# Optimization experiments

Measured on AMD Instinct MI355X. Metric: run time of the kernel, lower is better.

The kernel has to match this reference:

```python
import jax, jax.numpy as jnp
import numpy as np

B, N, IN_DIM, DIM, HEADS = 2, 4096, 1024, 1024, 8
MAX_MASK = 2048
SCALE = DIM ** -0.5  # original uses full dim, not per-head dim


def setup_inputs() -> dict:
    key = jax.random.key(0)
    k_x, k_qkv, k_o, k_b, k_m = jax.random.split(key, 5)
    x = jax.random.normal(k_x, (B, N, IN_DIM), dtype=jnp.float32)
    W_qkv = jax.random.normal(k_qkv, (IN_DIM, 3 * DIM), dtype=jnp.float32) * 0.02
    W_out = jax.random.normal(k_o, (DIM, DIM), dtype=jnp.float32) * 0.02
    b_out = jax.random.normal(k_b, (DIM,), dtype=jnp.float32) * 0.02
    mask = jax.random.randint(k_m, (1, 1, MAX_MASK, MAX_MASK), 0, 2, dtype=jnp.int32)
    return {"x": x, "W_qkv": W_qkv, "W_out": W_out, "b_out": b_out,
            "mask": mask, "max_mask": MAX_MASK}


def reference(x, W_qkv, W_out, b_out, mask, max_mask):
    b, n, _ = x.shape
    d = DIM // HEADS
    qkv = x @ W_qkv                                   # [b, n, 3*dim]
    qkv = qkv.reshape(b, n, 3, HEADS, d).transpose(2, 0, 3, 1, 4)  # [3, b, h, n, d]
    q, k, v = qkv[0], qkv[1], qkv[2]
    dots = jnp.einsum('bhid,bhjd->bhij', q, k) * SCALE  # [b, h, n, n]
    # partial submatrix masking on the top-left [max_mask, max_mask] block
    m = max_mask
    sub = jnp.where(mask == 0, -jnp.inf, dots[:, :, :m, :m])
    dots = dots.at[:, :, :m, :m].set(sub)
    attn = jax.nn.softmax(dots, axis=-1)
    out = jnp.einsum('bhij,bhjd->bhid', attn, v)       # [b, h, n, d]
    out = out.transpose(0, 2, 1, 3).reshape(b, n, HEADS * d)
    return out @ W_out + b_out
```

## Files before the change

kernel.cpp:

```cpp
#include <hip/hip_runtime.h>
#include <hip/hip_bf16.h>
#include <stdint.h>


typedef __attribute__((ext_vector_type(8))) short short8;
typedef __attribute__((ext_vector_type(4))) float f32x4;
typedef __attribute__((ext_vector_type(16))) float f32x16;
typedef unsigned int uint2v __attribute__((ext_vector_type(2)));

#define SCALE_Q 0.0450842200f

__device__ __forceinline__ unsigned short f2bf(float f) {
  union { float f; unsigned int u; } v;
  v.f = f;
  return (unsigned short)((v.u + 0x7fffu + ((v.u >> 16) & 1u)) >> 16);
}

__device__ __forceinline__ unsigned int pkbf2(float a, float b) {
  __hip_bfloat162 h = __float22bfloat162_rn(make_float2(a, b));
  union { __hip_bfloat162 h; unsigned int u; } c;
  c.h = h;
  return c.u;
}

__device__ __forceinline__ void gload_lds16(const void* g, void* l) {
  __builtin_amdgcn_global_load_lds(
      (const __attribute__((address_space(1))) uint32_t*)(uintptr_t)g,
      (__attribute__((address_space(3))) uint32_t*)(uintptr_t)l, 16, 0, 0);
}

__device__ __forceinline__ f32x4 zero4() {
  f32x4 z; z.x = 0.f; z.y = 0.f; z.z = 0.f; z.w = 0.f; return z;
}

__global__ __launch_bounds__(256) void k_cvt_x(const float* __restrict__ in,
                                               unsigned short* __restrict__ out) {
  const int t = blockIdx.x * 256 + threadIdx.x;
  const float4 v = ((const float4*)in)[t];
  ushort4 o;
  o.x = f2bf(v.x); o.y = f2bf(v.y); o.z = f2bf(v.z); o.w = f2bf(v.w);
  ((ushort4*)out)[t] = o;
}

__global__ __launch_bounds__(256) void k_cvt_wt(const float* __restrict__ w,
                                                unsigned short* __restrict__ wt,
                                                int Nn) {
  __shared__ float t[32][33];
  const int n0 = blockIdx.x << 5, k0 = blockIdx.y << 5;
  const int c = threadIdx.x & 31, r8 = threadIdx.x >> 5;
#pragma unroll
  for (int i = 0; i < 4; ++i) {
    const int r = (i << 3) + r8;
    t[r][c] = w[(long)(k0 + r) * Nn + n0 + c];
  }
  __syncthreads();
#pragma unroll
  for (int i = 0; i < 4; ++i) {
    const int r = (i << 3) + r8;
    wt[(long)(n0 + r) * 1024 + k0 + c] = f2bf(t[c][r]);
  }
}

__global__ __launch_bounds__(256) void k_mask_bits(
    const int* __restrict__ m, unsigned long long* __restrict__ mb) {
  const int t = blockIdx.x * 256 + threadIdx.x;
  const unsigned long long b = __ballot(m[t] != 0);
  if ((threadIdx.x & 63) == 0) mb[t >> 6] = b;
}

__global__ __launch_bounds__(256, 2) void k_qkv_gemm(
    const unsigned short* __restrict__ A,
    const unsigned short* __restrict__ Bt,
    unsigned short* __restrict__ Qs, unsigned short* __restrict__ Ks,
    unsigned short* __restrict__ Vt) {
  __shared__ __align__(16) unsigned short lA[8][128][8];
  __shared__ __align__(16) unsigned short lB[8][128][8];
  const int tid = threadIdx.x;
  const int w = tid >> 6, ln = tid & 63;
  const int m15 = ln & 15, q4 = ln >> 4;
  const int wm = (w >> 1) << 6, wn = (w & 1) << 6;
  const int id = blockIdx.x;
  const int swz = (id & 7) * 192 + (id >> 3);
  const int tn = swz % 24, tm = swz / 24;
  const int which = tn >> 3;
  const int h = tn & 7;

  f32x4 acc[4][4];
#pragma unroll
  for (int i = 0; i < 4; ++i)
#pragma unroll
    for (int j = 0; j < 4; ++j) acc[i][j] = zero4();

#define QKV_STAGE()                                                       \
  {                                                                       \
    _Pragma("unroll")                                                     \
    for (int c = 0; c < 4; ++c) {                                         \
      const int p = ((c * 4 + w) << 10) + (ln << 4);                      \
      const int g = p >> 11;                                              \
      const int r = (p & 2047) >> 4;                                      \
      gload_lds16(A + ((long)tm * 128 + r) * 1024 + kb + g * 8,           \
                  (char*)&lA[0][0][0] + p);                               \
      gload_lds16(Bt + ((long)tn * 128 + r) * 1024 + kb + g * 8,          \
                  (char*)&lB[0][0][0] + p);                               \
    }                                                                     \
  }

  if (which == 2) {
    for (int kb = 0; kb < 1024; kb += 64) {
      __syncthreads();
      QKV_STAGE();
      __syncthreads();
#pragma unroll
      for (int kk = 0; kk < 2; ++kk) {
        short8 afr[4], bfr[4];
#pragma unroll
        for (int i = 0; i < 4; ++i)
          afr[i] = *(const short8*)&lA[kk * 4 + q4][wm + i * 16 + m15][0];
#pragma unroll
        for (int j = 0; j < 4; ++j)
          bfr[j] = *(const short8*)&lB[kk * 4 + q4][wn + j * 16 + m15][0];
#pragma unroll
        for (int i = 0; i < 4; ++i)
#pragma unroll
          for (int j = 0; j < 4; ++j)
            acc[i][j] = __builtin_amdgcn_mfma_f32_16x16x32_bf16(
                afr[i], bfr[j], acc[i][j], 0, 0, 0);
      }
    }
#pragma unroll
    for (int i = 0; i < 4; ++i) {
      const int m0 = (tm << 7) + wm + (i << 4) + (q4 << 2);
      const int b = m0 >> 12, row0 = m0 & 4095;
#pragma unroll
      for (int j = 0; j < 4; ++j) {
        const int dd = wn + (j << 4) + m15;
        const long bh = b * 8 + h;
        uint2 u;
        u.x = pkbf2(acc[i][j][0], acc[i][j][1]);
        u.y = pkbf2(acc[i][j][2], acc[i][j][3]);
        *(uint2*)&Vt[(bh * 128 + dd) * 4096 + row0] = u;
      }
    }
  } else {
    for (int kb = 0; kb < 1024; kb += 64) {
      __syncthreads();
      QKV_STAGE();
      __syncthreads();
#pragma unroll
      for (int kk = 0; kk < 2; ++kk) {
        short8 afr[4], bfr[4];
#pragma unroll
        for (int i = 0; i < 4; ++i)
          afr[i] = *(const short8*)&lA[kk * 4 + q4][wm + i * 16 + m15][0];
#pragma unroll
        for (int j = 0; j < 4; ++j)
          bfr[j] = *(const short8*)&lB[kk * 4 + q4][wn + j * 16 + m15][0];
#pragma unroll
        for (int i = 0; i < 4; ++i)
#pragma unroll
          for (int j = 0; j < 4; ++j)
            acc[i][j] = __builtin_amdgcn_mfma_f32_16x16x32_bf16(
                bfr[j], afr[i], acc[i][j], 0, 0, 0);
      }
    }
    unsigned short* Dst = (which == 0) ? Qs : Ks;
    const float sc = (which == 0) ? SCALE_Q : 1.0f;
#pragma unroll
    for (int i = 0; i < 4; ++i) {
      const int m = (tm << 7) + wm + (i << 4) + m15;
      const int b = m >> 12, row = m & 4095;
      const long bh = b * 8 + h;
#pragma unroll
      for (int j = 0; j < 4; ++j) {
        const int dd0 = wn + (j << 4) + (q4 << 2);
        uint2 u;
        u.x = pkbf2(acc[i][j][0] * sc, acc[i][j][1] * sc);
        u.y = pkbf2(acc[i][j][2] * sc, acc[i][j][3] * sc);
        *(uint2*)&Dst[(bh * 4096 + row) * 128 + dd0] = u;
      }
    }
  }
#undef QKV_STAGE
}

__global__ __launch_bounds__(256, 2) void k_flash(
    const unsigned short* __restrict__ Qs, const unsigned short* __restrict__ Ks,
    const unsigned short* __restrict__ Vt,
    const unsigned long long* __restrict__ mbits,
    unsigned short* __restrict__ Ob) {
  __shared__ __align__(16) unsigned short lK[2][16][64][8];
  __shared__ __align__(16) unsigned short lV[2][8][128][8];

  const int tid = threadIdx.x;
  const int w = tid >> 6, ln = tid & 63;
  const int l31 = ln & 31, hi = ln >> 5, hi4 = hi << 2;
  const bool hib = hi != 0;
  (void)hib;
  const int id = blockIdx.x;
  const int xcd = id & 7, jj = id >> 3;
  const int bh = (xcd << 1) | (jj >> 5);
  const int rowblk = jj & 31;
  const int rbase = rowblk * 128 + w * 32;
  const int qrow = rbase + l31;

  const unsigned short* Qbh = Qs + (long)bh * 524288;
  const unsigned short* Kbh = Ks + (long)bh * 524288;
  const unsigned short* Vbh = Vt + (long)bh * 524288;

  short8 qf[8];
#pragma unroll
  for (int ks = 0; ks < 8; ++ks)
    qf[ks] = *(const short8*)(Qbh + (long)qrow * 128 + ks * 16 + hi * 8);

  f32x16 o[4];
#pragma unroll
  for (int d = 0; d < 4; ++d)
#pragma unroll
    for (int r = 0; r < 16; ++r) o[d][r] = 0.f;
  float lacc = 0.f;

  const bool maskblk = rowblk < 16;

#define STAGE_KV(dst, kvoff)                                              \
  {                                                                       \
    _Pragma("unroll")                                                     \
    for (int c = 0; c < 4; ++c) {                                         \
      const int p = ((c * 4 + w) << 10) + (ln << 4);                      \
      const int cs = p >> 10;                                             \
      const int j = (p & 1023) >> 4;                                      \
      gload_lds16(Kbh + (long)((kvoff) + j) * 128 + cs * 8,               \
                  (char*)&lK[dst][0][0][0] + p);                          \
    }                                                                     \
    _Pragma("unroll")                                                     \
    for (int c = 0; c < 4; ++c) {                                         \
      const int p = ((c * 4 + w) << 10) + (ln << 4);                      \
      const int cv = p >> 11;                                             \
      const int dv = (p & 2047) >> 4;                                     \
      gload_lds16(Vbh + (long)dv * 4096 + (kvoff) + cv * 8,               \
                  (char*)&lV[dst][0][0][0] + p);                          \
    }                                                                     \
  }

#if __has_builtin(__builtin_amdgcn_permlane32_swap)
#define PLSWAP(a, b)                                                      \
  {                                                                       \
    uint2v r_ = __builtin_amdgcn_permlane32_swap((a), (b), false, false); \
    (a) = r_[0]; (b) = r_[1];                                             \
  }
#else
#define PLSWAP(a, b)                                                      \
  {                                                                       \
    const unsigned pa_ = (unsigned)__shfl_xor((int)(a), 32);              \
    const unsigned pb_ = (unsigned)__shfl_xor((int)(b), 32);              \
    const unsigned na_ = hib ? pb_ : (a);                                 \
    const unsigned nb_ = hib ? (b) : pa_;                                 \
    (a) = na_; (b) = nb_;                                                 \
  }
#endif

  STAGE_KV(0, 0);
  __syncthreads();

  int cur = 0;
  for (int kv = 0; kv < 4096; kv += 64) {
    unsigned long long mw = 0ull;
    const bool domask = maskblk && (kv < 2048);
    if (domask) mw = mbits[(long)qrow * 32 + (kv >> 6)];

    const int nb = cur ^ 1;
    if (kv + 64 < 4096) STAGE_KV(nb, kv + 64);

    f32x16 s0, s1;
#pragma unroll
    for (int r = 0; r < 16; ++r) { s0[r] = 0.f; s1[r] = 0.f; }
    __builtin_amdgcn_s_setprio(1);
#pragma unroll
    for (int ks = 0; ks < 8; ++ks) {
      const short8 kf0 = *(const short8*)&lK[cur][ks * 2 + hi][l31][0];
      const short8 kf1 = *(const short8*)&lK[cur][ks * 2 + hi][32 + l31][0];
      s0 = __builtin_amdgcn_mfma_f32_32x32x16_bf16(kf0, qf[ks], s0, 0, 0, 0);
      s1 = __builtin_amdgcn_mfma_f32_32x32x16_bf16(kf1, qf[ks], s1, 0, 0, 0);
    }
    __builtin_amdgcn_s_setprio(0);

    if (domask) {
      const unsigned mlo = ((unsigned)mw) >> hi4;
      const unsigned mhi = ((unsigned)(mw >> 32)) >> hi4;
#pragma unroll
      for (int r = 0; r < 16; ++r) {
        const int c = ((r >> 2) << 3) + (r & 3);
        if (!((mlo >> c) & 1u)) s0[r] = -1e30f;
        if (!((mhi >> c) & 1u)) s1[r] = -1e30f;
      }
    }

    float p0[16], p1[16];
#pragma unroll
    for (int r = 0; r < 16; ++r) {
      p0[r] = __builtin_amdgcn_exp2f(s0[r]);
      p1[r] = __builtin_amdgcn_exp2f(s1[r]);
      lacc += p0[r] + p1[r];
    }

    unsigned w00 = pkbf2(p0[0], p0[1]),   w01 = pkbf2(p0[2], p0[3]);
    unsigned w10 = pkbf2(p0[4], p0[5]),   w11 = pkbf2(p0[6], p0[7]);
    PLSWAP(w00, w10); PLSWAP(w01, w11);
    unsigned w20 = pkbf2(p0[8], p0[9]),   w21 = pkbf2(p0[10], p0[11]);
    unsigned w30 = pkbf2(p0[12], p0[13]), w31 = pkbf2(p0[14], p0[15]);
    PLSWAP(w20, w30); PLSWAP(w21, w31);
    unsigned x00 = pkbf2(p1[0], p1[1]),   x01 = pkbf2(p1[2], p1[3]);
    unsigned x10 = pkbf2(p1[4], p1[5]),   x11 = pkbf2(p1[6], p1[7]);
    PLSWAP(x00, x10); PLSWAP(x01, x11);
    unsigned x20 = pkbf2(p1[8], p1[9]),   x21 = pkbf2(p1[10], p1[11]);
    unsigned x30 = pkbf2(p1[12], p1[13]), x31 = pkbf2(p1[14], p1[15]);
    PLSWAP(x20, x30); PLSWAP(x21, x31);

    union { unsigned u[4]; short8 s; } pa0, pa1, pa2, pa3;
    pa0.u[0] = w00; pa0.u[1] = w01; pa0.u[2] = w10; pa0.u[3] = w11;
    pa1.u[0] = w20; pa1.u[1] = w21; pa1.u[2] = w30; pa1.u[3] = w31;
    pa2.u[0] = x00; pa2.u[1] = x01; pa2.u[2] = x10; pa2.u[3] = x11;
    pa3.u[0] = x20; pa3.u[1] = x21; pa3.u[2] = x30; pa3.u[3] = x31;
    const short8 pa[4] = {pa0.s, pa1.s, pa2.s, pa3.s};

    __builtin_amdgcn_s_setprio(1);
#pragma unroll
    for (int ksl = 0; ksl < 4; ++ksl) {
#pragma unroll
      for (int db = 0; db < 4; ++db) {
        const short8 vf =
            *(const short8*)&lV[cur][ksl * 2 + hi][db * 32 + l31][0];
        o[db] = __builtin_amdgcn_mfma_f32_32x32x16_bf16(pa[ksl], vf,
                                                        o[db], 0, 0, 0);
      }
    }
    __builtin_amdgcn_s_setprio(0);

    __syncthreads();
    cur = nb;
  }
#undef STAGE_KV
#undef PLSWAP

  const float lh = lacc + __shfl_xor(lacc, 32);
  const float linv = 1.0f / lh;

  const int b = bh >> 3, h = bh & 7;
#pragma unroll
  for (int r = 0; r < 16; ++r) {
    const int qr = (r & 3) + ((r >> 2) << 3) + hi4;
    const float li = __shfl(linv, qr);
    const int row = rbase + qr;
    unsigned short* op = Ob + ((long)(b * 4096 + row)) * 1024 + h * 128 + l31;
#pragma unroll
    for (int db = 0; db < 4; ++db)
      op[db * 32] = f2bf(o[db][r] * li);
  }
}

__global__ __launch_bounds__(256, 2) void k_proj_gemm(
    const unsigned short* __restrict__ A,
    const unsigned short* __restrict__ Bt,
    const float* __restrict__ bias, float* __restrict__ Out) {
  __shared__ __align__(16) unsigned short lA[8][128][8];
  __shared__ __align__(16) unsigned short lB[8][128][8];
  const int tid = threadIdx.x;
  const int w = tid >> 6, ln = tid & 63;
  const int m15 = ln & 15, q4 = ln >> 4;
  const int wm = (w >> 1) << 6, wn = (w & 1) << 6;
  const int id = blockIdx.x;
  const int swz = (id & 7) * 64 + (id >> 3);
  const int tn = swz & 7, tm = swz >> 3;

  f32x4 acc[4][4];
#pragma unroll
  for (int i = 0; i < 4; ++i)
#pragma unroll
    for (int j = 0; j < 4; ++j) acc[i][j] = zero4();

  for (int kb = 0; kb < 1024; kb += 64) {
    __syncthreads();
#pragma unroll
    for (int c = 0; c < 4; ++c) {
      const int p = ((c * 4 + w) << 10) + (ln << 4);
      const int g = p >> 11;
      const int r = (p & 2047) >> 4;
      gload_lds16(A + ((long)tm * 128 + r) * 1024 + kb + g * 8,
                  (char*)&lA[0][0][0] + p);
      gload_lds16(Bt + ((long)tn * 128 + r) * 1024 + kb + g * 8,
                  (char*)&lB[0][0][0] + p);
    }
    __syncthreads();
#pragma unroll
    for (int kk = 0; kk < 2; ++kk) {
      short8 afr[4], bfr[4];
#pragma unroll
      for (int i = 0; i < 4; ++i)
        afr[i] = *(const short8*)&lA[kk * 4 + q4][wm + i * 16 + m15][0];
#pragma unroll
      for (int j = 0; j < 4; ++j)
        bfr[j] = *(const short8*)&lB[kk * 4 + q4][wn + j * 16 + m15][0];
#pragma unroll
      for (int i = 0; i < 4; ++i)
#pragma unroll
        for (int j = 0; j < 4; ++j)
          acc[i][j] = __builtin_amdgcn_mfma_f32_16x16x32_bf16(
              afr[i], bfr[j], acc[i][j], 0, 0, 0);
    }
  }

#pragma unroll
  for (int i = 0; i < 4; ++i)
#pragma unroll
    for (int r = 0; r < 4; ++r) {
      const int m = (tm << 7) + wm + (i << 4) + (q4 << 2) + r;
#pragma unroll
      for (int j = 0; j < 4; ++j) {
        const int n = (tn << 7) + wn + (j << 4) + m15;
        Out[(long)m * 1024 + n] = acc[i][j][r] + bias[n];
      }
    }
}

extern "C" void kernel_launch(void* const* d_in, const int* in_sizes, int n_in,
                              void* d_out, int out_size, void* d_ws,
                              size_t ws_size, hipStream_t stream) {
  const float* x = (const float*)d_in[0];
  const float* Wqkv = (const float*)d_in[1];
  const float* Wout = (const float*)d_in[2];
  const float* bout = (const float*)d_in[3];
  const int* mask = (const int*)d_in[4];
  float* out = (float*)d_out;

  char* ws = (char*)d_ws;
  unsigned short* xb     = (unsigned short*)(ws);
  unsigned short* wqkv_t = (unsigned short*)(ws + 16777216);
  unsigned short* wout_t = (unsigned short*)(ws + 23068672);
  unsigned short* Qs     = (unsigned short*)(ws + 25165824);
  unsigned short* Ks     = (unsigned short*)(ws + 41943040);
  unsigned short* Vt     = (unsigned short*)(ws + 58720256);
  unsigned short* Ob     = xb;
  unsigned long long* mbits = (unsigned long long*)wqkv_t;

  hipLaunchKernelGGL(k_cvt_x, dim3(8192), dim3(256), 0, stream, x, xb);
  hipLaunchKernelGGL(k_cvt_wt, dim3(96, 32), dim3(256), 0, stream, Wqkv, wqkv_t, 3072);
  hipLaunchKernelGGL(k_cvt_wt, dim3(32, 32), dim3(256), 0, stream, Wout, wout_t, 1024);
  hipLaunchKernelGGL(k_qkv_gemm, dim3(1536), dim3(256), 0, stream,
                     xb, wqkv_t, Qs, Ks, Vt);
  hipLaunchKernelGGL(k_mask_bits, dim3(16384), dim3(256), 0, stream,
                     mask, mbits);
  hipLaunchKernelGGL(k_flash, dim3(512), dim3(256), 0, stream,
                     Qs, Ks, Vt, mbits, Ob);
  hipLaunchKernelGGL(k_proj_gemm, dim3(512), dim3(256), 0, stream,
                     Ob, wout_t, bout, out);
}
```

Before: 431.2 us.

## Double-buffer GEMM LDS tiles, split flash PV into halves, merge prep kernels

Three conversion kernels are merged into one launch to cut launch overhead. Both the QKV and projection GEMMs now double-buffer their LDS tiles, prefetching the next K slice while MFMAs run on the current one, which drops one barrier per iteration. In the flash kernel, the softmax/exp/pack of the second 32-column half is interleaved with the PV MFMAs of the first half, so VALU work can overlap matrix work. Doubling LDS per GEMM block may lower occupancy under launch_bounds(256,2).

Result: no change. 426.2 us (-1.2%).

```diff
diff --git a/kernel.cpp b/kernel.cpp
--- a/kernel.cpp
+++ b/kernel.cpp
@@ -33,31 +33,43 @@
   f32x4 z; z.x = 0.f; z.y = 0.f; z.z = 0.f; z.w = 0.f; return z;
 }
 
-__global__ __launch_bounds__(256) void k_cvt_x(const float* __restrict__ in,
-                                               unsigned short* __restrict__ out) {
-  const int t = blockIdx.x * 256 + threadIdx.x;
-  const float4 v = ((const float4*)in)[t];
-  ushort4 o;
-  o.x = f2bf(v.x); o.y = f2bf(v.y); o.z = f2bf(v.z); o.w = f2bf(v.w);
-  ((ushort4*)out)[t] = o;
-}
-
-__global__ __launch_bounds__(256) void k_cvt_wt(const float* __restrict__ w,
-                                                unsigned short* __restrict__ wt,
-                                                int Nn) {
+__global__ __launch_bounds__(256) void k_prep(
+    const float* __restrict__ x, unsigned short* __restrict__ xb,
+    const float* __restrict__ Wqkv, unsigned short* __restrict__ wqkv_t,
+    const float* __restrict__ Wout, unsigned short* __restrict__ wout_t) {
   __shared__ float t[32][33];
-  const int n0 = blockIdx.x << 5, k0 = blockIdx.y << 5;
-  const int c = threadIdx.x & 31, r8 = threadIdx.x >> 5;
-#pragma unroll
-  for (int i = 0; i < 4; ++i) {
-    const int r = (i << 3) + r8;
-    t[r][c] = w[(long)(k0 + r) * Nn + n0 + c];
-  }
-  __syncthreads();
-#pragma unroll
-  for (int i = 0; i < 4; ++i) {
-    const int r = (i << 3) + r8;
-    wt[(long)(n0 + r) * 1024 + k0 + c] = f2bf(t[c][r]);
+  const int id = blockIdx.x;
+  const int tid = threadIdx.x;
+  if (id < 8192) {
+    const int i = id * 256 + tid;
+    const float4 v = ((const float4*)x)[i];
+    ushort4 o;
+    o.x = f2bf(v.x); o.y = f2bf(v.y); o.z = f2bf(v.z); o.w = f2bf(v.w);
+    ((ushort4*)xb)[i] = o;
+  } else {
+    const float* w;
+    unsigned short* wt;
+    int Nn, bx, by;
+    if (id < 11264) {
+      const int r = id - 8192;
+      w = Wqkv; wt = wqkv_t; Nn = 3072; bx = r % 96; by = r / 96;
+    } else {
+      const int r = id - 11264;
+      w = Wout; wt = wout_t; Nn = 1024; bx = r % 32; by = r / 32;
+    }
+    const int n0 = bx << 5, k0 = by << 5;
+    const int c = tid & 31, r8 = tid >> 5;
+#pragma unroll
+    for (int i = 0; i < 4; ++i) {
+      const int r = (i << 3) + r8;
+      t[r][c] = w[(long)(k0 + r) * Nn + n0 + c];
+    }
+    __syncthreads();
+#pragma unroll
+    for (int i = 0; i < 4; ++i) {
+      const int r = (i << 3) + r8;
+      wt[(long)(n0 + r) * 1024 + k0 + c] = f2bf(t[c][r]);
+    }
   }
 }
 
@@ -73,8 +85,8 @@
     const unsigned short* __restrict__ Bt,
     unsigned short* __restrict__ Qs, unsigned short* __restrict__ Ks,
     unsigned short* __restrict__ Vt) {
-  __shared__ __align__(16) unsigned short lA[8][128][8];
-  __shared__ __align__(16) unsigned short lB[8][128][8];
+  __shared__ __align__(16) unsigned short lA[2][8][128][8];
+  __shared__ __align__(16) unsigned short lB[2][8][128][8];
   const int tid = threadIdx.x;
   const int w = tid >> 6, ln = tid & 63;
   const int m15 = ln & 15, q4 = ln >> 4;
@@ -91,34 +103,37 @@
 #pragma unroll
     for (int j = 0; j < 4; ++j) acc[i][j] = zero4();
 
-#define QKV_STAGE()                                                       \
+#define QKV_STAGE(buf, kb)                                                \
   {                                                                       \
     _Pragma("unroll")                                                     \
     for (int c = 0; c < 4; ++c) {                                         \
       const int p = ((c * 4 + w) << 10) + (ln << 4);                      \
       const int g = p >> 11;                                              \
       const int r = (p & 2047) >> 4;                                      \
-      gload_lds16(A + ((long)tm * 128 + r) * 1024 + kb + g * 8,           \
-                  (char*)&lA[0][0][0] + p);                               \
-      gload_lds16(Bt + ((long)tn * 128 + r) * 1024 + kb + g * 8,          \
-                  (char*)&lB[0][0][0] + p);                               \
+      gload_lds16(A + ((long)tm * 128 + r) * 1024 + (kb) + g * 8,         \
+                  (char*)&lA[buf][0][0][0] + p);                          \
+      gload_lds16(Bt + ((long)tn * 128 + r) * 1024 + (kb) + g * 8,        \
+                  (char*)&lB[buf][0][0][0] + p);                          \
     }                                                                     \
   }
 
+  QKV_STAGE(0, 0);
+  __syncthreads();
+
+  int cur = 0;
   if (which == 2) {
     for (int kb = 0; kb < 1024; kb += 64) {
-      __syncthreads();
-      QKV_STAGE();
-      __syncthreads();
+      const int nb2 = cur ^ 1;
+      if (kb + 64 < 1024) QKV_STAGE(nb2, kb + 64);
 #pragma unroll
       for (int kk = 0; kk < 2; ++kk) {
         short8 afr[4], bfr[4];
 #pragma unroll
         for (int i = 0; i < 4; ++i)
-          afr[i] = *(const short8*)&lA[kk * 4 + q4][wm + i * 16 + m15][0];
+          afr[i] = *(const short8*)&lA[cur][kk * 4 + q4][wm + i * 16 + m15][0];
 #pragma unroll
         for (int j = 0; j < 4; ++j)
-          bfr[j] = *(const short8*)&lB[kk * 4 + q4][wn + j * 16 + m15][0];
+          bfr[j] = *(const short8*)&lB[cur][kk * 4 + q4][wn + j * 16 + m15][0];
 #pragma unroll
         for (int i = 0; i < 4; ++i)
 #pragma unroll
@@ -126,6 +141,8 @@
             acc[i][j] = __builtin_amdgcn_mfma_f32_16x16x32_bf16(
                 afr[i], bfr[j], acc[i][j], 0, 0, 0);
       }
+      __syncthreads();
+      cur = nb2;
     }
 #pragma unroll
     for (int i = 0; i < 4; ++i) {
@@ -143,18 +160,17 @@
     }
   } else {
     for (int kb = 0; kb < 1024; kb += 64) {
-      __syncthreads();
-      QKV_STAGE();
-      __syncthreads();
+      const int nb2 = cur ^ 1;
+      if (kb + 64 < 1024) QKV_STAGE(nb2, kb + 64);
 #pragma unroll
       for (int kk = 0; kk < 2; ++kk) {
         short8 afr[4], bfr[4];
 #pragma unroll
         for (int i = 0; i < 4; ++i)
-          afr[i] = *(const short8*)&lA[kk * 4 + q4][wm + i * 16 + m15][0];
+          afr[i] = *(const short8*)&lA[cur][kk * 4 + q4][wm + i * 16 + m15][0];
 #pragma unroll
         for (int j = 0; j < 4; ++j)
-          bfr[j] = *(const short8*)&lB[kk * 4 + q4][wn + j * 16 + m15][0];
+          bfr[j] = *(const short8*)&lB[cur][kk * 4 + q4][wn + j * 16 + m15][0];
 #pragma unroll
         for (int i = 0; i < 4; ++i)
 #pragma unroll
@@ -162,6 +178,8 @@
             acc[i][j] = __builtin_amdgcn_mfma_f32_16x16x32_bf16(
                 bfr[j], afr[i], acc[i][j], 0, 0, 0);
       }
+      __syncthreads();
+      cur = nb2;
     }
     unsigned short* Dst = (which == 0) ? Qs : Ks;
     const float sc = (which == 0) ? SCALE_Q : 1.0f;
@@ -283,55 +301,72 @@
     }
     __builtin_amdgcn_s_setprio(0);
 
+    const unsigned mlo = ((unsigned)mw) >> hi4;
+    const unsigned mhi = ((unsigned)(mw >> 32)) >> hi4;
+
     if (domask) {
-      const unsigned mlo = ((unsigned)mw) >> hi4;
-      const unsigned mhi = ((unsigned)(mw >> 32)) >> hi4;
 #pragma unroll
       for (int r = 0; r < 16; ++r) {
         const int c = ((r >> 2) << 3) + (r & 3);
         if (!((mlo >> c) & 1u)) s0[r] = -1e30f;
-        if (!((mhi >> c) & 1u)) s1[r] = -1e30f;
-      }
-    }
-
-    float p0[16], p1[16];
+      }
+    }
+    float p0[16];
 #pragma unroll
     for (int r = 0; r < 16; ++r) {
       p0[r] = __builtin_amdgcn_exp2f(s0[r]);
-      p1[r] = __builtin_amdgcn_exp2f(s1[r]);
-      lacc += p0[r] + p1[r];
-    }
-
+      lacc += p0[r];
+    }
     unsigned w00 = pkbf2(p0[0], p0[1]),   w01 = pkbf2(p0[2], p0[3]);
     unsigned w10 = pkbf2(p0[4], p0[5]),   w11 = pkbf2(p0[6], p0[7]);
     PLSWAP(w00, w10); PLSWAP(w01, w11);
     unsigned w20 = pkbf2(p0[8], p0[9]),   w21 = pkbf2(p0[10], p0[11]);
     unsigned w30 = pkbf2(p0[12], p0[13]), w31 = pkbf2(p0[14], p0[15]);
     PLSWAP(w20, w30); PLSWAP(w21, w31);
+    union { unsigned u[4]; short8 s; } pa0, pa1;
+    pa0.u[0] = w00; pa0.u[1] = w01; pa0.u[2] = w10; pa0.u[3] = w11;
+    pa1.u[0] = w20; pa1.u[1] = w21; pa1.u[2] = w30; pa1.u[3] = w31;
+
+    __builtin_amdgcn_s_setprio(1);
+#pragma unroll
+    for (int db = 0; db < 4; ++db) {
+      const short8 vf0 = *(const short8*)&lV[cur][hi][db * 32 + l31][0];
+      o[db] = __builtin_amdgcn_mfma_f32_32x32x16_bf16(pa0.s, vf0, o[db], 0, 0, 0);
+      const short8 vf1 = *(const short8*)&lV[cur][2 + hi][db * 32 + l31][0];
+      o[db] = __builtin_amdgcn_mfma_f32_32x32x16_bf16(pa1.s, vf1, o[db], 0, 0, 0);
+    }
+    __builtin_amdgcn_s_setprio(0);
+
+    if (domask) {
+#pragma unroll
+      for (int r = 0; r < 16; ++r) {
+        const int c = ((r >> 2) << 3) + (r & 3);
+        if (!((mhi >> c) & 1u)) s1[r] = -1e30f;
+      }
+    }
+    float p1[16];
+#pragma unroll
+    for (int r = 0; r < 16; ++r) {
+      p1[r] = __builtin_amdgcn_exp2f(s1[r]);
+      lacc += p1[r];
+    }
     unsigned x00 = pkbf2(p1[0], p1[1]),   x01 = pkbf2(p1[2], p1[3]);
     unsigned x10 = pkbf2(p1[4], p1[5]),   x11 = pkbf2(p1[6], p1[7]);
     PLSWAP(x00, x10); PLSWAP(x01, x11);
     unsigned x20 = pkbf2(p1[8], p1[9]),   x21 = pkbf2(p1[10], p1[11]);
     unsigned x30 = pkbf2(p1[12], p1[13]), x31 = pkbf2(p1[14], p1[15]);
     PLSWAP(x20, x30); PLSWAP(x21, x31);
-
-    union { unsigned u[4]; short8 s; } pa0, pa1, pa2, pa3;
-    pa0.u[0] = w00; pa0.u[1] = w01; pa0.u[2] = w10; pa0.u[3] = w11;
-    pa1.u[0] = w20; pa1.u[1] = w21; pa1.u[2] = w30; pa1.u[3] = w31;
+    union { unsigned u[4]; short8 s; } pa2, pa3;
     pa2.u[0] = x00; pa2.u[1] = x01; pa2.u[2] = x10; pa2.u[3] = x11;
     pa3.u[0] = x20; pa3.u[1] = x21; pa3.u[2] = x30; pa3.u[3] = x31;
-    const short8 pa[4] = {pa0.s, pa1.s, pa2.s, pa3.s};
 
     __builtin_amdgcn_s_setprio(1);
 #pragma unroll
-    for (int ksl = 0; ksl < 4; ++ksl) {
-#pragma unroll
-      for (int db = 0; db < 4; ++db) {
-        const short8 vf =
-            *(const short8*)&lV[cur][ksl * 2 + hi][db * 32 + l31][0];
-        o[db] = __builtin_amdgcn_mfma_f32_32x32x16_bf16(pa[ksl], vf,
-                                                        o[db], 0, 0, 0);
-      }
+    for (int db = 0; db < 4; ++db) {
+      const short8 vf2 = *(const short8*)&lV[cur][4 + hi][db * 32 + l31][0];
+      o[db] = __builtin_amdgcn_mfma_f32_32x32x16_bf16(pa2.s, vf2, o[db], 0, 0, 0);
+      const short8 vf3 = *(const short8*)&lV[cur][6 + hi][db * 32 + l31][0];
+      o[db] = __builtin_amdgcn_mfma_f32_32x32x16_bf16(pa3.s, vf3, o[db], 0, 0, 0);
     }
     __builtin_amdgcn_s_setprio(0);
 
@@ -361,8 +396,8 @@
     const unsigned short* __restrict__ A,
     const unsigned short* __restrict__ Bt,
     const float* __restrict__ bias, float* __restrict__ Out) {
-  __shared__ __align__(16) unsigned short lA[8][128][8];
-  __shared__ __align__(16) unsigned short lB[8][128][8];
+  __shared__ __align__(16) unsigned short lA[2][8][128][8];
+  __shared__ __align__(16) unsigned short lB[2][8][128][8];
   const int tid = threadIdx.x;
   const int w = tid >> 6, ln = tid & 63;
   const int m15 = ln & 15, q4 = ln >> 4;
@@ -377,28 +412,36 @@
 #pragma unroll
     for (int j = 0; j < 4; ++j) acc[i][j] = zero4();
 
+#define PROJ_STAGE(buf, kb)                                               \
+  {                                                                       \
+    _Pragma("unroll")                                                     \
+    for (int c = 0; c < 4; ++c) {                                         \
+      const int p = ((c * 4 + w) << 10) + (ln << 4);                      \
+      const int g = p >> 11;                                              \
+      const int r = (p & 2047) >> 4;                                      \
+      gload_lds16(A + ((long)tm * 128 + r) * 1024 + (kb) + g * 8,         \
+                  (char*)&lA[buf][0][0][0] + p);                          \
+      gload_lds16(Bt + ((long)tn * 128 + r) * 1024 + (kb) + g * 8,        \
+                  (char*)&lB[buf][0][0][0] + p);                          \
+    }                                                                     \
+  }
+
+  PROJ_STAGE(0, 0);
+  __syncthreads();
+
+  int cur = 0;
   for (int kb = 0; kb < 1024; kb += 64) {
-    __syncthreads();
-#pragma unroll
-    for (int c = 0; c < 4; ++c) {
-      const int p = ((c * 4 + w) << 10) + (ln << 4);
-      const int g = p >> 11;
-      const int r = (p & 2047) >> 4;
-      gload_lds16(A + ((long)tm * 128 + r) * 1024 + kb + g * 8,
-                  (char*)&lA[0][0][0] + p);
-      gload_lds16(Bt + ((long)tn * 128 + r) * 1024 + kb + g * 8,
-                  (char*)&lB[0][0][0] + p);
-    }
-    __syncthreads();
+    const int nb2 = cur ^ 1;
+    if (kb + 64 < 1024) PROJ_STAGE(nb2, kb + 64);
 #pragma unroll
     for (int kk = 0; kk < 2; ++kk) {
       short8 afr[4], bfr[4];
 #pragma unroll
       for (int i = 0; i < 4; ++i)
-        afr[i] = *(const short8*)&lA[kk * 4 + q4][wm + i * 16 + m15][0];
+        afr[i] = *(const short8*)&lA[cur][kk * 4 + q4][wm + i * 16 + m15][0];
 #pragma unroll
       for (int j = 0; j < 4; ++j)
-        bfr[j] = *(const short8*)&lB[kk * 4 + q4][wn + j * 16 + m15][0];
+        bfr[j] = *(const short8*)&lB[cur][kk * 4 + q4][wn + j * 16 + m15][0];
 #pragma unroll
       for (int i = 0; i < 4; ++i)
 #pragma unroll
@@ -406,7 +449,10 @@
           acc[i][j] = __builtin_amdgcn_mfma_f32_16x16x32_bf16(
               afr[i], bfr[j], acc[i][j], 0, 0, 0);
     }
-  }
+    __syncthreads();
+    cur = nb2;
+  }
+#undef PROJ_STAGE
 
 #pragma unroll
   for (int i = 0; i < 4; ++i)
@@ -441,9 +487,8 @@
   unsigned short* Ob     = xb;
   unsigned long long* mbits = (unsigned long long*)wqkv_t;
 
-  hipLaunchKernelGGL(k_cvt_x, dim3(8192), dim3(256), 0, stream, x, xb);
-  hipLaunchKernelGGL(k_cvt_wt, dim3(96, 32), dim3(256), 0, stream, Wqkv, wqkv_t, 3072);
-  hipLaunchKernelGGL(k_cvt_wt, dim3(32, 32), dim3(256), 0, stream, Wout, wout_t, 1024);
+  hipLaunchKernelGGL(k_prep, dim3(12288), dim3(256), 0, stream,
+                     x, xb, Wqkv, wqkv_t, Wout, wout_t);
   hipLaunchKernelGGL(k_qkv_gemm, dim3(1536), dim3(256), 0, stream,
                      xb, wqkv_t, Qs, Ks, Vt);
   hipLaunchKernelGGL(k_mask_bits, dim3(16384), dim3(256), 0, stream,
```
